# Kernel optimization log

Hardware: AMD Instinct MI355X
Metric: run time of the kernel (lower is better)

## Reference

```python
import jax, jax.numpy as jnp
import numpy as np

B, S, T, H, VS, VE = 32, 128, 128, 512, 8000, 8000


def _lstm_scan(x_proj, W_hh, bias, h0, c0):
    # x_proj: [L, B, 4H] precomputed input projections; gate order i,f,g,o (PyTorch)
    def step(carry, xp):
        h, c = carry
        gates = xp + h @ W_hh.T + bias  # [B, 4H]
        i, f, g, o = jnp.split(gates, 4, axis=-1)
        c = jax.nn.sigmoid(f) * c + jax.nn.sigmoid(i) * jnp.tanh(g)
        h = jax.nn.sigmoid(o) * jnp.tanh(c)
        return (h, c), h
    (h, c), hs = jax.lax.scan(step, (h0, c0), x_proj)
    return hs, h, c


def setup_inputs() -> dict:
    key = jax.random.key(0)
    ks = jax.random.split(key, 16)
    sc_h = 1.0 / np.sqrt(H)
    u = lambda k, shape: jax.random.uniform(k, shape, jnp.float32, -sc_h, sc_h)
    return {
        "input_batch": jax.random.randint(ks[0], (B, S), 0, VS),
        "output_batch": jax.random.randint(ks[1], (B, T), 0, VE),
        "Wa": u(ks[2], (H, H)), "ba": u(ks[3], (H,)),
        "W1": u(ks[4], (H, 2 * H)), "b1": u(ks[5], (H,)),
        "W2": u(ks[6], (VE, H)), "b2": u(ks[7], (VE,)),
        "We_ih": u(ks[8], (4 * H, VS)), "We_hh": u(ks[9], (4 * H, H)),
        "be_ih": u(ks[10], (4 * H,)), "be_hh": u(ks[11], (4 * H,)),
        "Wd_ih": u(ks[12], (4 * H, VE)), "Wd_hh": u(ks[13], (4 * H, H)),
        "bd_ih": u(ks[14], (4 * H,)), "bd_hh": u(ks[15], (4 * H,)),
    }


def reference(input_batch, output_batch, Wa, ba, W1, b1, W2, b2,
              We_ih, We_hh, be_ih, be_hh, Wd_ih, Wd_hh, bd_ih, bd_hh):
    src = input_batch.T  # [S, B]
    tgt = output_batch.T  # [T, B]
    # one_hot(tok) @ W_ih.T  ==  W_ih.T[tok]  (gather instead of dense one-hot GEMM)
    enc_xp = jnp.take(We_ih.T, src, axis=0)  # [S, B, 4H]
    dec_xp = jnp.take(Wd_ih.T, tgt, axis=0)  # [T, B, 4H]
    h0 = jnp.zeros((B, H), jnp.float32)
    c0 = jnp.zeros((B, H), jnp.float32)
    enc_outputs, h, c = _lstm_scan(enc_xp, We_hh, be_ih + be_hh, h0, c0)  # [S,B,H]
    proj_enc = enc_outputs @ Wa.T + ba  # attn(enc_outputs): [S, B, H]
    dec_bias = bd_ih + bd_hh

    def dec_step(carry, xp):
        h, c = carry
        gates = xp + h @ Wd_hh.T + dec_bias
        i, f, g, o = jnp.split(gates, 4, axis=-1)
        c = jax.nn.sigmoid(f) * c + jax.nn.sigmoid(i) * jnp.tanh(g)
        h = jax.nn.sigmoid(o) * jnp.tanh(c)  # [B, H] == dec_output
        scores = jnp.einsum('sbh,bh->bs', proj_enc, h)  # [B, S]
        w = jax.nn.softmax(scores, axis=1)
        context = jnp.einsum('bs,sbh->bh', w, enc_outputs)  # [B, H]
        hid = jnp.tanh(jnp.concatenate([h, context], axis=1) @ W1.T + b1)
        logits = hid @ W2.T + b2  # [B, VE]
        return (h, c), logits

    _, model = jax.lax.scan(dec_step, (h, c), dec_xp)  # [T, B, VE]
    return jax.nn.softmax(model.transpose(1, 0, 2), axis=2)  # [B, T, VE]
```

## Files before the change

### kernel.cpp

```cpp
#include <hip/hip_runtime.h>
#include <hip/hip_cooperative_groups.h>

#define NB 32
#define NS 128
#define NT 128
#define NH 512
#define NVS 8000
#define NVE 8000

typedef float fx4 __attribute__((ext_vector_type(4)));

__device__ __forceinline__ float sigm(float x) { return 1.0f / (1.0f + expf(-x)); }

__device__ __forceinline__ fx4 load_cg(const float* p) {
  fx4 v;
  asm volatile("global_load_dwordx4 %0, %1, off sc0 sc1" : "=v"(v) : "v"(p));
  return v;
}
__device__ __forceinline__ void store_cg(float* p, fx4 v) {
  asm volatile("global_store_dwordx4 %0, %1, off sc0 sc1" :: "v"(p), "v"(v) : "memory");
}

__global__ __launch_bounds__(256) void scan_kernel(
    const int* __restrict__ in_tok, const int* __restrict__ out_tok,
    const float* __restrict__ We_ih, const float* __restrict__ We_hh,
    const float* __restrict__ be_ih, const float* __restrict__ be_hh,
    const float* __restrict__ Wd_ih, const float* __restrict__ Wd_hh,
    const float* __restrict__ bd_ih, const float* __restrict__ bd_hh,
    float* __restrict__ h_buf,
    float* __restrict__ enc_out,
    float* __restrict__ dec_h,
    int* __restrict__ flags)
{
  __shared__ float W_lds[16][520];
  __shared__ float h_lds[16 * 516];
  __shared__ float gbuf[16][16];
  __shared__ float c_buf[4][16];
  __shared__ float hstage[16][4];

  const int tid = threadIdx.x;
  const int g   = blockIdx.x;
  const int bg  = g & 1;
  const int mg  = g >> 1;
  const int r   = tid >> 4;
  const int bl  = tid & 15;
  const int b   = bg * 16 + bl;
  const int q   = r >> 2;
  const int i   = r & 3;
  const int j   = q * NH + mg * 4 + i;

  const float bias_e = be_ih[j] + be_hh[j];
  const float bias_d = bd_ih[j] + bd_hh[j];
  const float* Wcol_e = We_ih + (size_t)j * NVS;
  const float* Wcol_d = Wd_ih + (size_t)j * NVE;

  if (tid < 64) c_buf[tid >> 4][tid & 15] = 0.0f;

  {
    const float* Wg = We_hh;
    for (int u = tid; u < 2048; u += 256) {
      const int rr = u >> 7;
      const int k4 = (u & 127) << 2;
      const int jj = (rr >> 2) * NH + mg * 4 + (rr & 3);
      *(float4*)&W_lds[rr][k4] = *(const float4*)(Wg + (size_t)jj * NH + k4);
    }
  }
  __syncthreads();

  for (int s = 0; s < NS + NT; ++s) {
    const bool enc = (s < NS);
    if (s == NS) {
      const float* Wg = Wd_hh;
      for (int u = tid; u < 2048; u += 256) {
        const int rr = u >> 7;
        const int k4 = (u & 127) << 2;
        const int jj = (rr >> 2) * NH + mg * 4 + (rr & 3);
        *(float4*)&W_lds[rr][k4] = *(const float4*)(Wg + (size_t)jj * NH + k4);
      }
      __syncthreads();
    }
    const int st  = enc ? s : s - NS;
    const int tok = enc ? in_tok[b * NS + st] : out_tok[b * NT + st];
    const float xp = enc ? Wcol_e[tok] : Wcol_d[tok];
    const float bias = enc ? bias_e : bias_d;
    const float* Wrow = &W_lds[r][0];

    float acc = 0.0f;
    if (s > 0) {
      if (tid < 128) {
        const int idx = (tid << 1) | bg;
        while (__hip_atomic_load(&flags[idx], __ATOMIC_RELAXED,
                                 __HIP_MEMORY_SCOPE_AGENT) < s)
          __builtin_amdgcn_s_sleep(1);
      }
      __syncthreads();
      const float* hsrc = h_buf + ((s - 1) & 1) * (NB * NH) + bg * 16 * NH;
      fx4 tmp[8];
      #pragma unroll
      for (int it = 0; it < 8; ++it)
        tmp[it] = load_cg(hsrc + ((tid + (it << 8)) << 2));
      asm volatile("s_waitcnt vmcnt(0)" ::: "memory");
      __builtin_amdgcn_sched_barrier(0);
      #pragma unroll
      for (int it = 0; it < 8; ++it) {
        const int u = tid + (it << 8);
        const int bb = u >> 7;
        const int kk = (u & 127) << 2;
        *(fx4*)&h_lds[bb * 516 + kk] = tmp[it];
      }
      __syncthreads();
      const float* hrow = &h_lds[bl * 516];
      #pragma unroll 8
      for (int k = 0; k < NH; k += 4) {
        const float4 hv = *(const float4*)(hrow + k);
        const float4 wv = *(const float4*)(Wrow + k);
        acc += hv.x * wv.x + hv.y * wv.y + hv.z * wv.z + hv.w * wv.w;
      }
    }
    gbuf[r][bl] = acc + xp + bias;
    __syncthreads();

    if (tid < 64) {
      const int ii = tid >> 4;
      const int bb = tid & 15;
      const float gi = gbuf[ii][bb];
      const float gf = gbuf[4 + ii][bb];
      const float gg = gbuf[8 + ii][bb];
      const float go = gbuf[12 + ii][bb];
      const float co = c_buf[ii][bb];
      const float cn = sigm(gf) * co + sigm(gi) * tanhf(gg);
      const float hn = sigm(go) * tanhf(cn);
      c_buf[ii][bb] = cn;
      hstage[bb][ii] = hn;
    }
    __syncthreads();
    if (tid < 16) {
      const fx4 hv = *(const fx4*)&hstage[tid][0];
      const int bglob = bg * 16 + tid;
      store_cg(h_buf + (s & 1) * (NB * NH) + bglob * NH + mg * 4, hv);
      float* dst = enc ? (enc_out + ((size_t)st * NB + bglob) * NH + mg * 4)
                       : (dec_h  + ((size_t)st * NB + bglob) * NH + mg * 4);
      *(fx4*)dst = hv;
    }
    asm volatile("s_waitcnt vmcnt(0)" ::: "memory");
    __syncthreads();
    if (tid == 0)
      __hip_atomic_store(&flags[g], s + 1, __ATOMIC_RELAXED,
                         __HIP_MEMORY_SCOPE_AGENT);
  }
}

template<int TRANSB, int CSWAP, int ACT>
__global__ __launch_bounds__(256) void gemm64(
    const float* __restrict__ A, const float* __restrict__ Bm,
    float* __restrict__ C, const float* __restrict__ bias,
    const float* __restrict__ A2, int ksplit,
    int M, int N, int K, int lda, int ldb, int ldc,
    long batchA, long batchB, long batchC)
{
  __shared__ float As[16][68];
  __shared__ float Bs[16][68];
  const int z = blockIdx.z;
  A += (long)z * batchA;
  if (A2 != nullptr) A2 += (long)z * batchA;
  Bm += (long)z * batchB;
  C  += (long)z * batchC;
  const int m0 = blockIdx.y << 6;
  const int n0 = blockIdx.x << 6;
  const int tid = threadIdx.x;
  const int tx = tid & 15;
  const int ty = tid >> 4;
  float acc[4][4] = {};

  for (int k0 = 0; k0 < K; k0 += 16) {
    {
      const int mrow = tid >> 2;
      const int kcq = (tid & 3) << 2;
      const float* base = A;
      int keff = k0;
      if (A2 != nullptr && k0 >= ksplit) { base = A2; keff = k0 - ksplit; }
      const float4 v = *(const float4*)(base + (long)(m0 + mrow) * lda + keff + kcq);
      As[kcq + 0][mrow] = v.x; As[kcq + 1][mrow] = v.y;
      As[kcq + 2][mrow] = v.z; As[kcq + 3][mrow] = v.w;
    }
    if (TRANSB == 0) {
      const int nrow = tid >> 2;
      const int kcq = (tid & 3) << 2;
      const float4 v = *(const float4*)(Bm + (long)(n0 + nrow) * ldb + k0 + kcq);
      Bs[kcq + 0][nrow] = v.x; Bs[kcq + 1][nrow] = v.y;
      Bs[kcq + 2][nrow] = v.z; Bs[kcq + 3][nrow] = v.w;
    } else {
      const int krow = tid >> 4;
      const int nc = (tid & 15) << 2;
      const float4 v = *(const float4*)(Bm + (long)(k0 + krow) * ldb + n0 + nc);
      *(float4*)&Bs[krow][nc] = v;
    }
    __syncthreads();
    #pragma unroll
    for (int kk = 0; kk < 16; ++kk) {
      const float4 a4 = *(const float4*)&As[kk][ty << 2];
      const float4 b4 = *(const float4*)&Bs[kk][tx << 2];
      const float a[4]  = {a4.x, a4.y, a4.z, a4.w};
      const float bv[4] = {b4.x, b4.y, b4.z, b4.w};
      #pragma unroll
      for (int ii = 0; ii < 4; ++ii)
        #pragma unroll
        for (int jj = 0; jj < 4; ++jj)
          acc[ii][jj] = fmaf(a[ii], bv[jj], acc[ii][jj]);
    }
    __syncthreads();
  }

  const int n = n0 + (tx << 2);
  float4 bb4 = {0.f, 0.f, 0.f, 0.f};
  if (bias) { bb4.x = bias[n]; bb4.y = bias[n + 1]; bb4.z = bias[n + 2]; bb4.w = bias[n + 3]; }
  #pragma unroll
  for (int ii = 0; ii < 4; ++ii) {
    const int mrow = m0 + (ty << 2) + ii;
    float4 o;
    o.x = acc[ii][0] + bb4.x; o.y = acc[ii][1] + bb4.y;
    o.z = acc[ii][2] + bb4.z; o.w = acc[ii][3] + bb4.w;
    if (ACT == 1) { o.x = tanhf(o.x); o.y = tanhf(o.y); o.z = tanhf(o.z); o.w = tanhf(o.w); }
    long orow = mrow;
    if (CSWAP) orow = (long)(mrow & (NB - 1)) * NT + (mrow >> 5);
    *(float4*)(C + orow * (long)ldc + n) = o;
  }
}

template<int CSWAP, int ACT>
__global__ __launch_bounds__(256) void gemm128db(
    const float* __restrict__ A, const float* __restrict__ Bm,
    float* __restrict__ C, const float* __restrict__ bias,
    const float* __restrict__ A2, int ksplit,
    int M, int N, int K, int lda, int ldb, int ldc)
{
  __shared__ float As[2][16][132];
  __shared__ float Bs[2][16][68];
  const int m0 = blockIdx.y << 7;
  const int n0 = blockIdx.x << 6;
  const int tid = threadIdx.x;
  const int tx = tid & 15;
  const int ty = tid >> 4;
  const int mrow = tid >> 1;
  const int kq   = (tid & 1) << 3;
  const int nrow = tid >> 2;
  const int kqb  = (tid & 3) << 2;
  float acc[8][4] = {};

  float4 va0, va1, vb;
  {
    const float* base = A;
    int keff = 0;
    if (A2 != nullptr && 0 >= ksplit) { base = A2; keff = -ksplit; }
    const float* p = base + (long)(m0 + mrow) * lda + keff + kq;
    va0 = *(const float4*)(p);
    va1 = *(const float4*)(p + 4);
    vb  = *(const float4*)(Bm + (long)(n0 + nrow) * ldb + kqb);
  }
  {
    As[0][kq + 0][mrow] = va0.x; As[0][kq + 1][mrow] = va0.y;
    As[0][kq + 2][mrow] = va0.z; As[0][kq + 3][mrow] = va0.w;
    As[0][kq + 4][mrow] = va1.x; As[0][kq + 5][mrow] = va1.y;
    As[0][kq + 6][mrow] = va1.z; As[0][kq + 7][mrow] = va1.w;
    Bs[0][kqb + 0][nrow] = vb.x; Bs[0][kqb + 1][nrow] = vb.y;
    Bs[0][kqb + 2][nrow] = vb.z; Bs[0][kqb + 3][nrow] = vb.w;
  }
  __syncthreads();

  const int T = K >> 4;
  for (int t = 0; t < T; ++t) {
    const int cur = t & 1;
    if (t + 1 < T) {
      const int k0 = (t + 1) << 4;
      const float* base = A;
      int keff = k0;
      if (A2 != nullptr && k0 >= ksplit) { base = A2; keff = k0 - ksplit; }
      const float* p = base + (long)(m0 + mrow) * lda + keff + kq;
      va0 = *(const float4*)(p);
      va1 = *(const float4*)(p + 4);
      vb  = *(const float4*)(Bm + (long)(n0 + nrow) * ldb + k0 + kqb);
    }
    #pragma unroll
    for (int kk = 0; kk < 16; ++kk) {
      const fx4 b4 = *(const fx4*)&Bs[cur][kk][tx << 2];
      const fx4 a0 = *(const fx4*)&As[cur][kk][ty << 3];
      const fx4 a1 = *(const fx4*)&As[cur][kk][(ty << 3) + 4];
      #pragma unroll
      for (int ii = 0; ii < 4; ++ii) {
        #pragma unroll
        for (int jj = 0; jj < 4; ++jj) {
          acc[ii][jj]     = fmaf(a0[ii], b4[jj], acc[ii][jj]);
          acc[ii + 4][jj] = fmaf(a1[ii], b4[jj], acc[ii + 4][jj]);
        }
      }
    }
    if (t + 1 < T) {
      const int nxt = cur ^ 1;
      As[nxt][kq + 0][mrow] = va0.x; As[nxt][kq + 1][mrow] = va0.y;
      As[nxt][kq + 2][mrow] = va0.z; As[nxt][kq + 3][mrow] = va0.w;
      As[nxt][kq + 4][mrow] = va1.x; As[nxt][kq + 5][mrow] = va1.y;
      As[nxt][kq + 6][mrow] = va1.z; As[nxt][kq + 7][mrow] = va1.w;
      Bs[nxt][kqb + 0][nrow] = vb.x; Bs[nxt][kqb + 1][nrow] = vb.y;
      Bs[nxt][kqb + 2][nrow] = vb.z; Bs[nxt][kqb + 3][nrow] = vb.w;
    }
    __syncthreads();
  }

  const int n = n0 + (tx << 2);
  float4 bb4 = {0.f, 0.f, 0.f, 0.f};
  if (bias) { bb4.x = bias[n]; bb4.y = bias[n + 1]; bb4.z = bias[n + 2]; bb4.w = bias[n + 3]; }
  #pragma unroll
  for (int ii = 0; ii < 8; ++ii) {
    const int mr = m0 + (ty << 3) + ii;
    float4 o;
    o.x = acc[ii][0] + bb4.x; o.y = acc[ii][1] + bb4.y;
    o.z = acc[ii][2] + bb4.z; o.w = acc[ii][3] + bb4.w;
    if (ACT == 1) { o.x = tanhf(o.x); o.y = tanhf(o.y); o.z = tanhf(o.z); o.w = tanhf(o.w); }
    long orow = mr;
    if (CSWAP) orow = (long)(mr & (NB - 1)) * NT + (mr >> 5);
    *(float4*)(C + orow * (long)ldc + n) = o;
  }
}

__global__ __launch_bounds__(128) void softmax_s(float* __restrict__ sc) {
  const long row = blockIdx.x;
  float* p = sc + row * NS;
  const float x = p[threadIdx.x];
  float mx = x;
  for (int o = 32; o; o >>= 1) mx = fmaxf(mx, __shfl_xor(mx, o));
  __shared__ float r0[2], r1[2];
  const int w = threadIdx.x >> 6;
  if ((threadIdx.x & 63) == 0) r0[w] = mx;
  __syncthreads();
  mx = fmaxf(r0[0], r0[1]);
  const float e = expf(x - mx);
  float sum = e;
  for (int o = 32; o; o >>= 1) sum += __shfl_xor(sum, o);
  if ((threadIdx.x & 63) == 0) r1[w] = sum;
  __syncthreads();
  sum = r1[0] + r1[1];
  p[threadIdx.x] = e / sum;
}

__global__ __launch_bounds__(256) void softmax_v(float* __restrict__ out) {
  const long row = blockIdx.x;
  float* p = out + row * NVE;
  float v[32];
  float mx = -1e30f;
  #pragma unroll
  for (int it = 0; it < 32; ++it) {
    const int idx = (it << 8) + threadIdx.x;
    v[it] = (idx < NVE) ? p[idx] : -1e30f;
    mx = fmaxf(mx, v[it]);
  }
  for (int o = 32; o; o >>= 1) mx = fmaxf(mx, __shfl_xor(mx, o));
  __shared__ float red[4], red2[4];
  const int w = threadIdx.x >> 6;
  if ((threadIdx.x & 63) == 0) red[w] = mx;
  __syncthreads();
  mx = fmaxf(fmaxf(red[0], red[1]), fmaxf(red[2], red[3]));
  float sum = 0.0f;
  #pragma unroll
  for (int it = 0; it < 32; ++it) {
    const int idx = (it << 8) + threadIdx.x;
    if (idx < NVE) { v[it] = expf(v[it] - mx); sum += v[it]; }
  }
  for (int o = 32; o; o >>= 1) sum += __shfl_xor(sum, o);
  if ((threadIdx.x & 63) == 0) red2[w] = sum;
  __syncthreads();
  sum = red2[0] + red2[1] + red2[2] + red2[3];
  const float inv = 1.0f / sum;
  #pragma unroll
  for (int it = 0; it < 32; ++it) {
    const int idx = (it << 8) + threadIdx.x;
    if (idx < NVE) p[idx] = v[it] * inv;
  }
}

extern "C" void kernel_launch(void* const* d_in, const int* in_sizes, int n_in,
                              void* d_out, int out_size, void* d_ws, size_t ws_size,
                              hipStream_t stream) {
  const int*   in_tok = (const int*)d_in[0];
  const int*   out_tok = (const int*)d_in[1];
  const float* Wa    = (const float*)d_in[2];
  const float* ba    = (const float*)d_in[3];
  const float* W1    = (const float*)d_in[4];
  const float* b1    = (const float*)d_in[5];
  const float* W2    = (const float*)d_in[6];
  const float* b2    = (const float*)d_in[7];
  const float* We_ih = (const float*)d_in[8];
  const float* We_hh = (const float*)d_in[9];
  const float* be_ih = (const float*)d_in[10];
  const float* be_hh = (const float*)d_in[11];
  const float* Wd_ih = (const float*)d_in[12];
  const float* Wd_hh = (const float*)d_in[13];
  const float* bd_ih = (const float*)d_in[14];
  const float* bd_hh = (const float*)d_in[15];

  float* ws      = (float*)d_ws;
  float* h_buf   = ws;
  float* enc_out = ws + 32768;
  float* dec_h   = ws + 2129920;
  float* proj    = ws + 4227072;
  float* scores  = ws + 6324224;
  float* ctx     = ws + 6848512;
  float* hid     = ws + 8945664;
  int*   flags   = (int*)(ws + 11042816);
  float* out     = (float*)d_out;

  (void)hipMemsetAsync((void*)flags, 0, 256 * sizeof(int), stream);

  {
    void* args[14];
    args[0] = (void*)&in_tok; args[1] = (void*)&out_tok;
    args[2] = (void*)&We_ih;  args[3] = (void*)&We_hh;
    args[4] = (void*)&be_ih;  args[5] = (void*)&be_hh;
    args[6] = (void*)&Wd_ih;  args[7] = (void*)&Wd_hh;
    args[8] = (void*)&bd_ih;  args[9] = (void*)&bd_hh;
    args[10] = (void*)&h_buf; args[11] = (void*)&enc_out; args[12] = (void*)&dec_h;
    args[13] = (void*)&flags;
    (void)hipLaunchCooperativeKernel((void*)scan_kernel, dim3(256), dim3(256), args, 0, stream);
  }

  gemm128db<0,0><<<dim3(8,32,1), 256, 0, stream>>>(
      enc_out, Wa, proj, ba, nullptr, 1 << 30,
      4096, 512, 512, 512, 512, 512);

  gemm64<0,0,0><<<dim3(2,2,NB), 256, 0, stream>>>(
      dec_h, proj, scores, nullptr, nullptr, 1 << 30,
      NT, NS, NH, NB * NH, NB * NH, NB * NS,
      (long)NH, (long)NH, (long)NS);

  softmax_s<<<dim3(NT * NB), 128, 0, stream>>>(scores);

  gemm64<1,0,0><<<dim3(8,2,NB), 256, 0, stream>>>(
      scores, enc_out, ctx, nullptr, nullptr, 1 << 30,
      NT, NH, NS, NB * NS, NB * NH, NB * NH,
      (long)NS, (long)NH, (long)NH);

  gemm128db<0,1><<<dim3(8,32,1), 256, 0, stream>>>(
      dec_h, W1, hid, b1, ctx, 512,
      4096, 512, 1024, 512, 1024, 512);

  gemm128db<1,0><<<dim3(125,32,1), 256, 0, stream>>>(
      hid, W2, out, b2, nullptr, 1 << 30,
      4096, NVE, 512, 512, 512, NVE);

  softmax_v<<<dim3(NB * NT), 256, 0, stream>>>(out);
}
```

Baseline: 2.235 ms.

## Compute logits GEMM with split-bf16 MFMA (3-pass hi/lo emulation of fp32)

Replaces the fp32 SIMT GEMM for the output-vocabulary logits with a matrix-core kernel. Both hid and W2 are first split into bf16 high and low parts, and the product is accumulated with three bf16 MFMA passes (hi*hi, hi*lo, lo*hi) to approximate fp32 accuracy. Dead workspace regions (proj, enc_out) are reused to hold the split operands. This adds two conversion kernels and extra global traffic. The new GEMM loads fragments straight from global memory with no LDS staging, so it may become bandwidth-bound.

After: 2.156 ms. -3.5%, faster.

```diff
diff --git a/kernel.cpp b/kernel.cpp
--- a/kernel.cpp
+++ b/kernel.cpp
@@ -9,6 +9,8 @@
 #define NVE 8000
 
 typedef float fx4 __attribute__((ext_vector_type(4)));
+typedef short bf16x8 __attribute__((ext_vector_type(8)));
+typedef float f32x4 __attribute__((ext_vector_type(4)));
 
 __device__ __forceinline__ float sigm(float x) { return 1.0f / (1.0f + expf(-x)); }
 
@@ -322,6 +324,98 @@
   }
 }
 
+__global__ __launch_bounds__(256) void split_bf16(
+    const float* __restrict__ x, unsigned short* __restrict__ hi,
+    unsigned short* __restrict__ lo, int n4)
+{
+  for (int i = blockIdx.x * 256 + threadIdx.x; i < n4; i += gridDim.x * 256) {
+    const float4 v = ((const float4*)x)[i];
+    float f[4] = {v.x, v.y, v.z, v.w};
+    unsigned short hh[4], ll[4];
+    #pragma unroll
+    for (int jj = 0; jj < 4; ++jj) {
+      const unsigned int u = __float_as_uint(f[jj]);
+      const unsigned int r = (u + 0x7FFFu + ((u >> 16) & 1u)) >> 16;
+      hh[jj] = (unsigned short)r;
+      const float hf = __uint_as_float(r << 16);
+      const float lf = f[jj] - hf;
+      const unsigned int u2 = __float_as_uint(lf);
+      const unsigned int r2 = (u2 + 0x7FFFu + ((u2 >> 16) & 1u)) >> 16;
+      ll[jj] = (unsigned short)r2;
+    }
+    ushort4 hv, lv;
+    hv.x = hh[0]; hv.y = hh[1]; hv.z = hh[2]; hv.w = hh[3];
+    lv.x = ll[0]; lv.y = ll[1]; lv.z = ll[2]; lv.w = ll[3];
+    ((ushort4*)hi)[i] = hv;
+    ((ushort4*)lo)[i] = lv;
+  }
+}
+
+__global__ __launch_bounds__(256) void gemm_mfma_logits(
+    const unsigned short* __restrict__ Ahi, const unsigned short* __restrict__ Alo,
+    const unsigned short* __restrict__ Bhi, const unsigned short* __restrict__ Blo,
+    float* __restrict__ C, const float* __restrict__ bias)
+{
+  const int tid  = threadIdx.x;
+  const int wid  = tid >> 6;
+  const int lane = tid & 63;
+  const int l15  = lane & 15;
+  const int kg   = lane >> 4;
+  const int m0   = (blockIdx.y << 7) + (wid << 5);
+  const int n0   = blockIdx.x << 6;
+
+  const size_t aoff = (size_t)(m0 + l15) * NH + (kg << 3);
+  const size_t boff = (size_t)(n0 + l15) * NH + (kg << 3);
+
+  f32x4 acc[2][4];
+  #pragma unroll
+  for (int fm = 0; fm < 2; ++fm)
+    #pragma unroll
+    for (int fn = 0; fn < 4; ++fn)
+      acc[fm][fn] = (f32x4){0.f, 0.f, 0.f, 0.f};
+
+  for (int k0 = 0; k0 < NH; k0 += 32) {
+    bf16x8 ah[2], al[2], bh[4], blv[4];
+    #pragma unroll
+    for (int fm = 0; fm < 2; ++fm) {
+      ah[fm] = *(const bf16x8*)(Ahi + aoff + (size_t)(fm << 4) * NH + k0);
+      al[fm] = *(const bf16x8*)(Alo + aoff + (size_t)(fm << 4) * NH + k0);
+    }
+    #pragma unroll
+    for (int fn = 0; fn < 4; ++fn) {
+      bh[fn]  = *(const bf16x8*)(Bhi + boff + (size_t)(fn << 4) * NH + k0);
+      blv[fn] = *(const bf16x8*)(Blo + boff + (size_t)(fn << 4) * NH + k0);
+    }
+    #pragma unroll
+    for (int fm = 0; fm < 2; ++fm) {
+      #pragma unroll
+      for (int fn = 0; fn < 4; ++fn) {
+        acc[fm][fn] = __builtin_amdgcn_mfma_f32_16x16x32_bf16(
+            ah[fm], bh[fn], acc[fm][fn], 0, 0, 0);
+        acc[fm][fn] = __builtin_amdgcn_mfma_f32_16x16x32_bf16(
+            ah[fm], blv[fn], acc[fm][fn], 0, 0, 0);
+        acc[fm][fn] = __builtin_amdgcn_mfma_f32_16x16x32_bf16(
+            al[fm], bh[fn], acc[fm][fn], 0, 0, 0);
+      }
+    }
+  }
+
+  #pragma unroll
+  for (int fm = 0; fm < 2; ++fm) {
+    #pragma unroll
+    for (int fn = 0; fn < 4; ++fn) {
+      const int n = n0 + (fn << 4) + l15;
+      const float bb = bias[n];
+      #pragma unroll
+      for (int rg = 0; rg < 4; ++rg) {
+        const int m = m0 + (fm << 4) + (kg << 2) + rg;
+        const long orow = (long)(m & (NB - 1)) * NT + (m >> 5);
+        C[orow * NVE + n] = acc[fm][fn][rg] + bb;
+      }
+    }
+  }
+}
+
 __global__ __launch_bounds__(128) void softmax_s(float* __restrict__ sc) {
   const long row = blockIdx.x;
   float* p = sc + row * NS;
@@ -408,6 +502,11 @@
   int*   flags   = (int*)(ws + 11042816);
   float* out     = (float*)d_out;
 
+  unsigned short* hid_hi = (unsigned short*)proj;
+  unsigned short* hid_lo = (unsigned short*)(proj + 1048576);
+  unsigned short* W2_hi  = (unsigned short*)enc_out;
+  unsigned short* W2_lo  = (unsigned short*)(enc_out + 2048000);
+
   (void)hipMemsetAsync((void*)flags, 0, 256 * sizeof(int), stream);
 
   {
@@ -442,9 +541,11 @@
       dec_h, W1, hid, b1, ctx, 512,
       4096, 512, 1024, 512, 1024, 512);
 
-  gemm128db<1,0><<<dim3(125,32,1), 256, 0, stream>>>(
-      hid, W2, out, b2, nullptr, 1 << 30,
-      4096, NVE, 512, 512, 512, NVE);
+  split_bf16<<<dim3(2048), 256, 0, stream>>>(hid, hid_hi, hid_lo, 4096 * 512 / 4);
+  split_bf16<<<dim3(2048), 256, 0, stream>>>(W2, W2_hi, W2_lo, NVE * 512 / 4);
+
+  gemm_mfma_logits<<<dim3(125, 32), 256, 0, stream>>>(
+      hid_hi, hid_lo, W2_hi, W2_lo, out, b2);
 
   softmax_v<<<dim3(NB * NT), 256, 0, stream>>>(out);
 }
```
